# Optimization experiments

Measured on AMD Instinct MI355X. Metric: run time of the kernel, lower is better.

The kernel has to match this reference:

```python
import jax, jax.numpy as jnp
from jax import lax
import numpy as np

EPS = 4e-3            # geoopt float32 ball boundary eps
MAXNORM = 1.0 - EPS   # c = 1 Poincare ball


def _norm(x):
    return jnp.sqrt(jnp.maximum(jnp.sum(x * x, axis=-1, keepdims=True), 1e-15))


def expmap0(u):
    n = _norm(u)
    return jnp.tanh(n) * u / n


def projx(x):
    n = _norm(x)
    return jnp.where(n > MAXNORM, x * (MAXNORM / n), x)


def mobius_add(x, y):
    x2 = jnp.sum(x * x, -1, keepdims=True)
    y2 = jnp.sum(y * y, -1, keepdims=True)
    xy = jnp.sum(x * y, -1, keepdims=True)
    num = (1.0 + 2.0 * xy + y2) * x + (1.0 - x2) * y
    den = 1.0 + 2.0 * xy + x2 * y2
    return num / jnp.maximum(den, 1e-15)


def mamba_layer(x, inW, convW, convb, xpW, dtW, dtb, A_log, Dp, outW):
    # x: [B,T,H]; inW: [2*Din,H]; convW: [Din,K]; xpW: [R+2N,Din]; dtW: [Din,R]
    B, T, H = x.shape
    Din, N = A_log.shape
    K = convW.shape[-1]
    R = dtW.shape[-1]
    xz = jnp.einsum('bth,dh->btd', x, inW)              # [B,T,2*Din]
    xr, z = jnp.split(xz, 2, axis=-1)
    xc = lax.conv_general_dilated(jnp.transpose(xr, (0, 2, 1)), convW[:, None, :],
                                  (1,), [(K - 1, 0)], feature_group_count=Din)
    u = jax.nn.silu(jnp.transpose(xc + convb[None, :, None], (0, 2, 1)))  # [B,T,Din]
    x_dbl = jnp.einsum('btd,ed->bte', u, xpW)           # [B,T,R+2N]
    dt_r, Bm, Cm = x_dbl[..., :R], x_dbl[..., R:R + N], x_dbl[..., R + N:]
    dt = jax.nn.softplus(jnp.einsum('btr,dr->btd', dt_r, dtW) + dtb)      # [B,T,Din]
    A = -jnp.exp(A_log)                                 # [Din,N]
    dA = jnp.exp(dt[..., None] * A)                     # [B,T,Din,N]
    dBu = dt[..., None] * Bm[:, :, None, :] * u[..., None]

    def step(h, ins):
        dA_t, dBu_t, C_t = ins
        h = dA_t * h + dBu_t                            # [B,Din,N]
        return h, jnp.einsum('bdn,bn->bd', h, C_t)

    h0 = jnp.zeros((B, Din, N), x.dtype)
    _, ys = lax.scan(step, h0, (jnp.moveaxis(dA, 1, 0), jnp.moveaxis(dBu, 1, 0), jnp.moveaxis(Cm, 1, 0)))
    y = jnp.moveaxis(ys, 0, 1) + Dp * u                 # [B,T,Din]
    return jnp.einsum('btd,hd->bth', y * jax.nn.silu(z), outW)


def _encode(xs, inp_W, inp_b, in_proj_W, conv_W, conv_b, xproj_W, dt_W, dt_b, A_log, D_skip, out_W, outp_W, outp_b):
    # xs: [4,B,T,1]; params carry leading branch dim 4, then layer dim 3
    def branch(x, iW, ib, ipW, cW, cb, xpW, dW, db, Al, Dp, oW, opW, opb):
        h = jnp.einsum('bti,hi->bth', x, iW) + ib
        for l in range(ipW.shape[0]):
            h = mamba_layer(h, ipW[l], cW[l], cb[l], xpW[l], dW[l], db[l], Al[l], Dp[l], oW[l])
        return jnp.tanh(jnp.einsum('bth,eh->bte', h, opW) + opb)
    return jax.vmap(branch)(xs, inp_W, inp_b, in_proj_W, conv_W, conv_b, xproj_W, dt_W, dt_b, A_log, D_skip, out_W, outp_W, outp_b)


def setup_inputs() -> dict:
    key = jax.random.key(0)
    ks = jax.random.split(key, 24)
    Br, B, T, H, Din, N, K, R, E, L = 4, 32, 1024, 64, 128, 16, 4, 4, 32, 3

    def rn(k, shape, s=0.05):
        return jax.random.normal(k, shape, jnp.float32) * s

    A_init = jnp.log(jnp.arange(1, N + 1, dtype=jnp.float32))
    return {
        'trend': jax.random.normal(ks[0], (B, T, 1), jnp.float32),
        'seasonal_weekly': jax.random.normal(ks[1], (B, T, 1), jnp.float32),
        'seasonal_daily': jax.random.normal(ks[2], (B, T, 1), jnp.float32),
        'residual': jax.random.normal(ks[3], (B, T, 1), jnp.float32),
        'inp_W': rn(ks[4], (Br, H, 1), 0.5),
        'inp_b': rn(ks[5], (Br, H)),
        'in_proj_W': rn(ks[6], (Br, L, 2 * Din, H)),
        'conv_W': rn(ks[7], (Br, L, Din, K), 0.2),
        'conv_b': rn(ks[8], (Br, L, Din)),
        'xproj_W': rn(ks[9], (Br, L, R + 2 * N, Din)),
        'dt_W': rn(ks[10], (Br, L, Din, R), 0.2),
        'dt_b': rn(ks[11], (Br, L, Din), 0.5) - 4.0,  # softplus(dt_b) small
        'A_log': jnp.tile(A_init, (Br, L, Din, 1)) + rn(ks[12], (Br, L, Din, N), 0.01),
        'D_skip': jnp.ones((Br, L, Din), jnp.float32) + rn(ks[13], (Br, L, Din), 0.01),
        'out_W': rn(ks[14], (Br, L, H, Din)),
        'outp_W': rn(ks[15], (Br, E, H)),
        'outp_b': rn(ks[16], (Br, E)),
    }


def reference(trend, seasonal_weekly, seasonal_daily, residual, inp_W, inp_b, in_proj_W, conv_W, conv_b, xproj_W, dt_W, dt_b, A_log, D_skip, out_W, outp_W, outp_b):
    xs = jnp.stack([trend, seasonal_weekly, seasonal_daily, residual], 0)  # [4,B,T,1]
    z = _encode(xs, inp_W, inp_b, in_proj_W, conv_W, conv_b, xproj_W, dt_W, dt_b, A_log, D_skip, out_W, outp_W, outp_b)  # [4,B,T,E]
    zh = projx(expmap0(z))
    t, w, d, r = zh[0], zh[1], zh[2], zh[3]
    comb = projx(mobius_add(mobius_add(t, mobius_add(w, d)), r))
    # stacked [trend_h, weekly_h, daily_h, residual_h, combined_h]
    return jnp.stack([t, w, d, r, comb], 0)
```

## Files before the change

kernel.cpp:

```cpp
#include <hip/hip_runtime.h>
#include <math.h>

#define TT 1024
#define DIN 128
#define HH 64
#define NN 16
#define EE 32
#define LL 3
#define BB 32

__device__ __forceinline__ float siluf(float x) { return x / (1.f + __expf(-x)); }

typedef __attribute__((ext_vector_type(8))) short bf16x8;
typedef __attribute__((ext_vector_type(4))) float f32x4;

__device__ __forceinline__ void split2(float x, ushort& hi, ushort& lo) {
  unsigned u = __float_as_uint(x);
  hi = (ushort)(u >> 16);
  float rem = x - __uint_as_float((u >> 16) << 16);
  lo = (ushort)(__float_as_uint(rem) >> 16);
}

__global__ __launch_bounds__(256) void k_xz(
    const float* __restrict__ x0, const float* __restrict__ x1,
    const float* __restrict__ x2, const float* __restrict__ x3,
    const float* __restrict__ h, const float* __restrict__ inprojW,
    const float* __restrict__ inpW, const float* __restrict__ inpb,
    float* __restrict__ xr, float* __restrict__ zb, int br0, int l) {
  __shared__ __align__(16) ushort Hh[64][72], Hl[64][72];
  __shared__ __align__(16) ushort Wh[64][72], Wl[64][72];
  const int tid = threadIdx.x;
  const int b  = blockIdx.y;
  const int t0 = blockIdx.x * 64;
  const int n0 = blockIdx.z * 64;
  const int br = br0 + (b >> 5);
  const float* Wg = inprojW + (size_t)((br * LL + l) * 2 * DIN + n0) * HH;
  const float* Hg = h + ((size_t)b * TT + t0) * HH;
  {
    int row = tid >> 2, c0 = (tid & 3) * 16;
    float xv = 0.f;
    if (l == 0) {
      int bb = b & 31;
      const float* xp = (br == 0) ? x0 : (br == 1) ? x1 : (br == 2) ? x2 : x3;
      xv = xp[bb * TT + t0 + row];
    }
    #pragma unroll
    for (int q = 0; q < 4; ++q) {
      float4 hv;
      if (l == 0) {
        float4 w4 = *(const float4*)(inpW + br * HH + c0 + q * 4);
        float4 b4 = *(const float4*)(inpb + br * HH + c0 + q * 4);
        hv.x = xv * w4.x + b4.x; hv.y = xv * w4.y + b4.y;
        hv.z = xv * w4.z + b4.z; hv.w = xv * w4.w + b4.w;
      } else {
        hv = *(const float4*)(Hg + (size_t)row * HH + c0 + q * 4);
      }
      ushort h0,h1,h2,h3,l0,l1,l2,l3;
      split2(hv.x,h0,l0); split2(hv.y,h1,l1); split2(hv.z,h2,l2); split2(hv.w,h3,l3);
      *(ushort4*)&Hh[row][c0 + q*4] = make_ushort4(h0,h1,h2,h3);
      *(ushort4*)&Hl[row][c0 + q*4] = make_ushort4(l0,l1,l2,l3);
      float4 wv = *(const float4*)(Wg + (size_t)row * HH + c0 + q * 4);
      split2(wv.x,h0,l0); split2(wv.y,h1,l1); split2(wv.z,h2,l2); split2(wv.w,h3,l3);
      *(ushort4*)&Wh[row][c0 + q*4] = make_ushort4(h0,h1,h2,h3);
      *(ushort4*)&Wl[row][c0 + q*4] = make_ushort4(l0,l1,l2,l3);
    }
  }
  __syncthreads();
  const int wave = tid >> 6, lane = tid & 63;
  const int quad = lane >> 4, l16 = lane & 15;
  const int nsub = (wave & 1) * 32, tsub = (wave >> 1) * 32;
  f32x4 acc[2][2] = {};
  #pragma unroll
  for (int k0 = 0; k0 < 64; k0 += 32) {
    bf16x8 Ah[2], Al[2], Bh[2], Bl[2];
    #pragma unroll
    for (int i = 0; i < 2; ++i) {
      Ah[i] = *(const bf16x8*)&Wh[nsub + i*16 + l16][k0 + quad*8];
      Al[i] = *(const bf16x8*)&Wl[nsub + i*16 + l16][k0 + quad*8];
      Bh[i] = *(const bf16x8*)&Hh[tsub + i*16 + l16][k0 + quad*8];
      Bl[i] = *(const bf16x8*)&Hl[tsub + i*16 + l16][k0 + quad*8];
    }
    #pragma unroll
    for (int i = 0; i < 2; ++i)
      #pragma unroll
      for (int j = 0; j < 2; ++j) {
        acc[i][j] = __builtin_amdgcn_mfma_f32_16x16x32_bf16(Ah[i], Bh[j], acc[i][j], 0, 0, 0);
        acc[i][j] = __builtin_amdgcn_mfma_f32_16x16x32_bf16(Ah[i], Bl[j], acc[i][j], 0, 0, 0);
        acc[i][j] = __builtin_amdgcn_mfma_f32_16x16x32_bf16(Al[i], Bh[j], acc[i][j], 0, 0, 0);
      }
  }
  #pragma unroll
  for (int i = 0; i < 2; ++i) {
    #pragma unroll
    for (int r = 0; r < 4; ++r) {
      int n = n0 + nsub + i*16 + quad*4 + r;
      float* dst = (n < DIN) ? (xr + ((size_t)b * DIN + n) * TT)
                             : (zb + ((size_t)b * DIN + (n - DIN)) * TT);
      #pragma unroll
      for (int j = 0; j < 2; ++j)
        dst[t0 + tsub + j*16 + l16] = acc[i][j][r];
    }
  }
}

__global__ __launch_bounds__(256) void k_xdbl(
    const float* __restrict__ xr, const float* __restrict__ convW,
    const float* __restrict__ convb, const float* __restrict__ xprojW,
    const float* __restrict__ dtW, const float* __restrict__ dtb,
    float* __restrict__ u, float* __restrict__ dt,
    float* __restrict__ Bm, float* __restrict__ Cm,
    int br0, int l) {
  __shared__ __align__(16) float Xr[16][72];
  __shared__ __align__(16) float As2[32][68];
  __shared__ __align__(16) float Ws2[32][48];
  __shared__ __align__(16) float Xs[40][68];
  const int tid = threadIdx.x;
  const int b  = blockIdx.y;
  const int t0 = blockIdx.x * 64;
  const int br = br0 + (b >> 5);
  const float* W = xprojW + (size_t)((br * LL + l) * 36) * DIN;
  const int rowk = tid >> 4, c4 = tid & 15;
  const int wave = tid >> 6, lane = tid & 63;
  const int quad = lane >> 4, l16 = lane & 15;
  const int tw = wave * 16;
  f32x4 acc[3] = {};
  for (int k0 = 0; k0 < DIN; k0 += 32) {
    #pragma unroll
    for (int ks = 0; ks < 32; ks += 16) {
      __syncthreads();
      {
        const float* src = xr + ((size_t)b * DIN + k0 + ks + rowk) * TT + t0;
        *(float4*)&Xr[rowk][4 + c4 * 4] = *(const float4*)(src + c4 * 4);
        if (tid < 16) {
          float4 hv = make_float4(0.f, 0.f, 0.f, 0.f);
          if (t0 > 0) hv = *(const float4*)(xr + ((size_t)b * DIN + k0 + ks + tid) * TT + t0 - 4);
          *(float4*)&Xr[tid][0] = hv;
        }
      }
      __syncthreads();
      {
        int d = k0 + ks + rowk;
        const float* w = convW + (size_t)((br * LL + l) * DIN + d) * 4;
        float w0 = w[0], w1 = w[1], w2 = w[2], w3 = w[3];
        float cb = convb[(br * LL + l) * DIN + d];
        int i0 = c4 * 4;
        float o[4];
        #pragma unroll
        for (int q = 0; q < 4; ++q) {
          int j = i0 + q;
          float a = Xr[rowk][j+1]*w0 + Xr[rowk][j+2]*w1 + Xr[rowk][j+3]*w2 + Xr[rowk][j+4]*w3 + cb;
          o[q] = siluf(a);
        }
        float4 uo = make_float4(o[0], o[1], o[2], o[3]);
        *(float4*)&As2[ks + rowk][i0] = uo;
        *(float4*)(u + ((size_t)b * DIN + d) * TT + t0 + i0) = uo;
      }
    }
    for (int idx = tid; idx < 1536; idx += 256) {
      int jj = idx >> 5, kk = idx & 31;
      Ws2[kk][jj] = (jj < 36) ? W[(size_t)jj * DIN + k0 + kk] : 0.f;
    }
    __syncthreads();
    ushort bh[8], bl[8];
    #pragma unroll
    for (int j = 0; j < 8; ++j) {
      float v = As2[quad * 8 + j][tw + l16];
      split2(v, bh[j], bl[j]);
    }
    bf16x8 Bh = *(bf16x8*)bh, Bl = *(bf16x8*)bl;
    #pragma unroll
    for (int nf = 0; nf < 3; ++nf) {
      ushort wh[8], wl[8];
      #pragma unroll
      for (int j = 0; j < 8; ++j) {
        float v = Ws2[quad * 8 + j][nf * 16 + l16];
        split2(v, wh[j], wl[j]);
      }
      bf16x8 Wh = *(bf16x8*)wh, Wl = *(bf16x8*)wl;
      acc[nf] = __builtin_amdgcn_mfma_f32_16x16x32_bf16(Wh, Bh, acc[nf], 0, 0, 0);
      acc[nf] = __builtin_amdgcn_mfma_f32_16x16x32_bf16(Wh, Bl, acc[nf], 0, 0, 0);
      acc[nf] = __builtin_amdgcn_mfma_f32_16x16x32_bf16(Wl, Bh, acc[nf], 0, 0, 0);
    }
  }
  __syncthreads();
  #pragma unroll
  for (int nf = 0; nf < 3; ++nf) {
    #pragma unroll
    for (int r = 0; r < 4; ++r) {
      int n = nf * 16 + quad * 4 + r;
      if (n < 40) Xs[n][tw + l16] = acc[nf][r];
    }
  }
  __syncthreads();
  {
    int n = tid >> 4, i0 = (tid & 15) * 4;
    *(float4*)(Bm + ((size_t)b * NN + n) * TT + t0 + i0) = *(float4*)&Xs[4 + n][i0];
    *(float4*)(Cm + ((size_t)b * NN + n) * TT + t0 + i0) = *(float4*)&Xs[20 + n][i0];
  }
  {
    int d = tid >> 1, half = tid & 1;
    const float* wd = dtW + (size_t)((br * LL + l) * DIN + d) * 4;
    float w0 = wd[0], w1 = wd[1], w2 = wd[2], w3 = wd[3];
    float bias = dtb[(br * LL + l) * DIN + d];
    float* dtp = dt + ((size_t)b * DIN + d) * TT + t0 + half * 32;
    #pragma unroll
    for (int g8 = 0; g8 < 8; ++g8) {
      float o[4];
      #pragma unroll
      for (int q = 0; q < 4; ++q) {
        int i = half * 32 + g8 * 4 + q;
        float s = Xs[0][i]*w0 + Xs[1][i]*w1 + Xs[2][i]*w2 + Xs[3][i]*w3 + bias;
        float e = __expf(-fabsf(s));
        o[q] = fmaxf(s, 0.f) + __logf(1.f + e);
      }
      *(float4*)(dtp + g8*4) = make_float4(o[0], o[1], o[2], o[3]);
    }
  }
}

__global__ __launch_bounds__(256) void k_scan1(
    float* dtc, const float* __restrict__ u,
    const float* __restrict__ Bm, const float* __restrict__ Cm,
    const float* __restrict__ A_log, const float* __restrict__ D_skip,
    float* __restrict__ Hloc, float* __restrict__ g, int br0, int l) {
  __shared__ __align__(16) float Bl[16][68];
  __shared__ __align__(16) float Cl[16][68];
  const int bx  = blockIdx.x;
  const int b   = bx >> 5;
  const int rem = bx & 31;
  const int c   = rem >> 1;
  const int dh  = rem & 1;
  const int tid = threadIdx.x;
  {
    int row = tid >> 4, cc = (tid & 15) * 4;
    *(float4*)&Bl[row][cc] = *(const float4*)(Bm + ((size_t)b * NN + row) * TT + c * 64 + cc);
    *(float4*)&Cl[row][cc] = *(const float4*)(Cm + ((size_t)b * NN + row) * TT + c * 64 + cc);
  }
  __syncthreads();
  const int d  = dh * 64 + (tid >> 2);
  const int n0 = (tid & 3) * 4;
  const int br = br0 + (b >> 5);
  const int wbase = (br * LL + l) * DIN + d;
  float Ac[4];
  #pragma unroll
  for (int j = 0; j < 4; ++j) Ac[j] = -__expf(A_log[(size_t)wbase * NN + n0 + j]);
  float Dp = D_skip[wbase];
  float* dtp = dtc + ((size_t)b * DIN + d) * TT + c * 64;
  const float* up = u + ((size_t)b * DIN + d) * TT + c * 64;
  float* gp = g + ((size_t)b * DIN + d) * TT + c * 64;
  float hst[4] = {0.f, 0.f, 0.f, 0.f};
  float sd = 0.f;
  for (int t0 = 0; t0 < 64; t0 += 8) {
    float4 dq0 = *(const float4*)(dtp + t0);
    float4 dq1 = *(const float4*)(dtp + t0 + 4);
    float4 uq0 = *(const float4*)(up + t0);
    float4 uq1 = *(const float4*)(up + t0 + 4);
    float dts[8] = {dq0.x, dq0.y, dq0.z, dq0.w, dq1.x, dq1.y, dq1.z, dq1.w};
    float us[8]  = {uq0.x, uq0.y, uq0.z, uq0.w, uq1.x, uq1.y, uq1.z, uq1.w};
    float Bs[4][8], Cr[4][8];
    #pragma unroll
    for (int j = 0; j < 4; ++j) {
      float4 b0 = *(const float4*)&Bl[n0 + j][t0];
      float4 b1 = *(const float4*)&Bl[n0 + j][t0 + 4];
      Bs[j][0]=b0.x; Bs[j][1]=b0.y; Bs[j][2]=b0.z; Bs[j][3]=b0.w;
      Bs[j][4]=b1.x; Bs[j][5]=b1.y; Bs[j][6]=b1.z; Bs[j][7]=b1.w;
      float4 c0 = *(const float4*)&Cl[n0 + j][t0];
      float4 c1 = *(const float4*)&Cl[n0 + j][t0 + 4];
      Cr[j][0]=c0.x; Cr[j][1]=c0.y; Cr[j][2]=c0.z; Cr[j][3]=c0.w;
      Cr[j][4]=c1.x; Cr[j][5]=c1.y; Cr[j][6]=c1.z; Cr[j][7]=c1.w;
    }
    float yo[8], cd8[8];
    #pragma unroll
    for (int s = 0; s < 8; ++s) {
      float dtv = dts[s], uv = us[s];
      sd += dtv;
      cd8[s] = sd;
      float du = dtv * uv;
      float acc = 0.f;
      #pragma unroll
      for (int j = 0; j < 4; ++j) {
        float dA = __expf(dtv * Ac[j]);
        hst[j] = dA * hst[j] + du * Bs[j][s];
        acc += hst[j] * Cr[j][s];
      }
      acc += __shfl_xor(acc, 1, 4);
      acc += __shfl_xor(acc, 2, 4);
      yo[s] = acc + Dp * uv;
    }
    if ((tid & 3) == 0) {
      *(float4*)(gp + t0)      = make_float4(yo[0], yo[1], yo[2], yo[3]);
      *(float4*)(gp + t0 + 4)  = make_float4(yo[4], yo[5], yo[6], yo[7]);
      *(float4*)(dtp + t0)     = make_float4(cd8[0], cd8[1], cd8[2], cd8[3]);
      *(float4*)(dtp + t0 + 4) = make_float4(cd8[4], cd8[5], cd8[6], cd8[7]);
    }
  }
  *(float4*)(Hloc + (((size_t)b * DIN + d) * 16 + c) * 16 + n0) =
      make_float4(hst[0], hst[1], hst[2], hst[3]);
}

__global__ __launch_bounds__(256) void k_scan2(
    const float* __restrict__ cd, const float* __restrict__ Cm,
    const float* __restrict__ A_log, const float* __restrict__ Hloc,
    float* __restrict__ g, int br0, int l) {
  __shared__ __align__(16) float Cl[16][68];
  __shared__ __align__(16) float HinL[32][16];
  const int bx  = blockIdx.x;
  const int b   = bx >> 6;
  const int rem = bx & 63;
  const int c   = rem >> 2;
  const int dq  = rem & 3;
  const int tid = threadIdx.x;
  const int br  = br0 + (b >> 5);
  if (c == 0) return;
  {
    int row = tid >> 4, cc = (tid & 15) * 4;
    *(float4*)&Cl[row][cc] = *(const float4*)(Cm + ((size_t)b * NN + row) * TT + c * 64 + cc);
  }
  {
    int dloc = tid >> 3;
    int n0 = (tid & 7) * 2;
    int d = dq * 32 + dloc;
    int wbase = (br * LL + l) * DIN + d;
    float a0 = -__expf(A_log[(size_t)wbase * NN + n0]);
    float a1 = -__expf(A_log[(size_t)wbase * NN + n0 + 1]);
    float h0 = 0.f, h1 = 0.f;
    const float* cdrow = cd + ((size_t)b * DIN + d) * TT;
    const float* hlb = Hloc + ((size_t)b * DIN + d) * 256;
    for (int cc = 0; cc < c; ++cc) {
      float sdv = cdrow[cc * 64 + 63];
      float2 hl = *(const float2*)(hlb + cc * 16 + n0);
      h0 = __expf(a0 * sdv) * h0 + hl.x;
      h1 = __expf(a1 * sdv) * h1 + hl.y;
    }
    HinL[dloc][n0] = h0;
    HinL[dloc][n0 + 1] = h1;
  }
  __syncthreads();
  const int dloc = tid >> 3, tg = tid & 7;
  const int d  = dq * 32 + dloc;
  const float* al = A_log + (size_t)((br * LL + l) * DIN + d) * NN;
  float Ac16[16];
  #pragma unroll
  for (int n = 0; n < 16; ++n) Ac16[n] = -__expf(al[n]);
  size_t off = ((size_t)b * DIN + d) * TT + c * 64 + tg * 8;
  float4 cd0 = *(const float4*)(cd + off);
  float4 cd1 = *(const float4*)(cd + off + 4);
  float cd8[8] = {cd0.x, cd0.y, cd0.z, cd0.w, cd1.x, cd1.y, cd1.z, cd1.w};
  float* gp = g + off;
  float4 y0 = *(float4*)gp;
  float4 y1 = *(float4*)(gp + 4);
  float y8[8] = {y0.x, y0.y, y0.z, y0.w, y1.x, y1.y, y1.z, y1.w};
  const int tbase = tg * 8;
  #pragma unroll
  for (int n = 0; n < 16; ++n) {
    float hv = HinL[dloc][n];
    float an = Ac16[n];
    #pragma unroll
    for (int s = 0; s < 8; ++s)
      y8[s] += Cl[n][tbase + s] * __expf(an * cd8[s]) * hv;
  }
  *(float4*)gp       = make_float4(y8[0], y8[1], y8[2], y8[3]);
  *(float4*)(gp + 4) = make_float4(y8[4], y8[5], y8[6], y8[7]);
}

__global__ __launch_bounds__(256) void k_out(
    const float* __restrict__ graw, const float* __restrict__ zb,
    const float* __restrict__ outW, float* __restrict__ h, int br0, int l) {
  __shared__ __align__(16) ushort Ah_[64][72], Al_[64][72];
  __shared__ __align__(16) ushort Bh_[64][72], Bl_[64][72];
  const int tid = threadIdx.x;
  const int b  = blockIdx.y;
  const int t0 = blockIdx.x * 64;
  const int br = br0 + (b >> 5);
  const float* Wg = outW + (size_t)((br * LL + l) * HH) * DIN;
  const int wave = tid >> 6, lane = tid & 63;
  const int quad = lane >> 4, l16 = lane & 15;
  const int hsub = (wave & 1) * 32, tsub = (wave >> 1) * 32;
  f32x4 acc[2][2] = {};
  for (int k0 = 0; k0 < DIN; k0 += 64) {
    __syncthreads();
    {
      int row = tid >> 2, c0 = (tid & 3) * 16;
      #pragma unroll
      for (int q = 0; q < 4; ++q) {
        float4 wv = *(const float4*)(Wg + (size_t)row * DIN + k0 + c0 + q * 4);
        ushort h0,h1,h2,h3,l0,l1,l2,l3;
        split2(wv.x,h0,l0); split2(wv.y,h1,l1); split2(wv.z,h2,l2); split2(wv.w,h3,l3);
        *(ushort4*)&Ah_[row][c0 + q*4] = make_ushort4(h0,h1,h2,h3);
        *(ushort4*)&Al_[row][c0 + q*4] = make_ushort4(l0,l1,l2,l3);
        size_t off = ((size_t)b * DIN + k0 + row) * TT + t0 + c0 + q * 4;
        float4 gv = *(const float4*)(graw + off);
        float4 zv = *(const float4*)(zb + off);
        float a0 = gv.x * siluf(zv.x), a1 = gv.y * siluf(zv.y);
        float a2 = gv.z * siluf(zv.z), a3 = gv.w * siluf(zv.w);
        split2(a0,h0,l0); split2(a1,h1,l1); split2(a2,h2,l2); split2(a3,h3,l3);
        *(ushort4*)&Bh_[row][c0 + q*4] = make_ushort4(h0,h1,h2,h3);
        *(ushort4*)&Bl_[row][c0 + q*4] = make_ushort4(l0,l1,l2,l3);
      }
    }
    __syncthreads();
    #pragma unroll
    for (int kk = 0; kk < 64; kk += 32) {
      bf16x8 Ahf[2], Alf[2], Bhf[2], Blf[2];
      #pragma unroll
      for (int i = 0; i < 2; ++i) {
        Ahf[i] = *(const bf16x8*)&Ah_[hsub + i*16 + l16][kk + quad*8];
        Alf[i] = *(const bf16x8*)&Al_[hsub + i*16 + l16][kk + quad*8];
        Bhf[i] = *(const bf16x8*)&Bh_[tsub + i*16 + l16][kk + quad*8];
        Blf[i] = *(const bf16x8*)&Bl_[tsub + i*16 + l16][kk + quad*8];
      }
      #pragma unroll
      for (int i = 0; i < 2; ++i)
        #pragma unroll
        for (int j = 0; j < 2; ++j) {
          acc[i][j] = __builtin_amdgcn_mfma_f32_16x16x32_bf16(Ahf[i], Bhf[j], acc[i][j], 0, 0, 0);
          acc[i][j] = __builtin_amdgcn_mfma_f32_16x16x32_bf16(Ahf[i], Blf[j], acc[i][j], 0, 0, 0);
          acc[i][j] = __builtin_amdgcn_mfma_f32_16x16x32_bf16(Alf[i], Bhf[j], acc[i][j], 0, 0, 0);
        }
    }
  }
  #pragma unroll
  for (int i = 0; i < 2; ++i) {
    int hh0 = hsub + i*16 + quad*4;
    #pragma unroll
    for (int j = 0; j < 2; ++j) {
      int t = t0 + tsub + j*16 + l16;
      *(f32x4*)(h + ((size_t)b * TT + t) * HH + hh0) = acc[i][j];
    }
  }
}

__global__ __launch_bounds__(256) void k_ze(
    const float* __restrict__ h, const float* __restrict__ outpW,
    const float* __restrict__ outpb, float* __restrict__ ze, int br0) {
  __shared__ __align__(16) float As[16][132];
  __shared__ __align__(16) float Ws[16][36];
  __shared__ __align__(16) float Cs[128][36];
  const int tid = threadIdx.x;
  const int b  = blockIdx.y;
  const int t0 = blockIdx.x * 128;
  const int br = br0 + (b >> 5);
  const float* W = outpW + (size_t)br * EE * HH;
  float acc[4][4] = {};
  const int ti = tid & 31, ni = tid >> 5;
  for (int k0 = 0; k0 < HH; k0 += 16) {
    __syncthreads();
    {
      int i = tid >> 1, kq = (tid & 1) * 8;
      const float* src = h + ((size_t)b * TT + t0 + i) * HH + k0 + kq;
      float4 a0 = *(const float4*)src;
      float4 a1 = *(const float4*)(src + 4);
      As[kq+0][i]=a0.x; As[kq+1][i]=a0.y; As[kq+2][i]=a0.z; As[kq+3][i]=a0.w;
      As[kq+4][i]=a1.x; As[kq+5][i]=a1.y; As[kq+6][i]=a1.z; As[kq+7][i]=a1.w;
    }
    for (int idx = tid; idx < 512; idx += 256) {
      int jj = idx >> 4, kk = idx & 15;
      Ws[kk][jj] = W[(size_t)jj * HH + k0 + kk];
    }
    __syncthreads();
    #pragma unroll
    for (int kk = 0; kk < 16; ++kk) {
      float4 a = *(const float4*)&As[kk][ti * 4];
      float4 w = *(const float4*)&Ws[kk][ni * 4];
      acc[0][0] += a.x*w.x; acc[0][1] += a.x*w.y; acc[0][2] += a.x*w.z; acc[0][3] += a.x*w.w;
      acc[1][0] += a.y*w.x; acc[1][1] += a.y*w.y; acc[1][2] += a.y*w.z; acc[1][3] += a.y*w.w;
      acc[2][0] += a.z*w.x; acc[2][1] += a.z*w.y; acc[2][2] += a.z*w.z; acc[2][3] += a.z*w.w;
      acc[3][0] += a.w*w.x; acc[3][1] += a.w*w.y; acc[3][2] += a.w*w.z; acc[3][3] += a.w*w.w;
    }
  }
  __syncthreads();
  float bj[4];
  #pragma unroll
  for (int c = 0; c < 4; ++c) bj[c] = outpb[br * EE + ni*4 + c];
  #pragma unroll
  for (int r = 0; r < 4; ++r)
    #pragma unroll
    for (int c = 0; c < 4; ++c)
      Cs[ti*4+r][ni*4+c] = tanhf(acc[r][c] + bj[c]);
  __syncthreads();
  int i = tid >> 1, j16 = (tid & 1) * 16;
  float* dst = ze + (((size_t)(br0 * 32 + b)) * TT + t0 + i) * EE + j16;
  #pragma unroll
  for (int q = 0; q < 4; ++q)
    *(float4*)(dst + q*4) = *(float4*)&Cs[i][j16 + q*4];
}

__device__ __forceinline__ void mobius_add32(const float* x, const float* y, float* o) {
  float x2 = 0.f, y2 = 0.f, xy = 0.f;
  #pragma unroll
  for (int i = 0; i < 32; ++i) { x2 += x[i]*x[i]; y2 += y[i]*y[i]; xy += x[i]*y[i]; }
  float ca  = 1.f + 2.f*xy + y2;
  float cb  = 1.f - x2;
  float den = 1.f + 2.f*xy + x2*y2;
  float inv = 1.f / fmaxf(den, 1e-15f);
  #pragma unroll
  for (int i = 0; i < 32; ++i) o[i] = (ca*x[i] + cb*y[i]) * inv;
}

__global__ __launch_bounds__(256) void k_hyper(const float* __restrict__ ze,
                                               float* __restrict__ out) {
  int idx = blockIdx.x * 256 + threadIdx.x;
  int b = idx >> 10, t = idx & 1023;
  float v[4][32];
  #pragma unroll
  for (int br = 0; br < 4; ++br) {
    const float* p = ze + (((size_t)br * BB + b) * TT + t) * EE;
    float s = 0.f;
    #pragma unroll
    for (int e = 0; e < 32; ++e) { v[br][e] = p[e]; s += v[br][e]*v[br][e]; }
    float nr = sqrtf(fmaxf(s, 1e-15f));
    float sc = tanhf(nr) / nr;
    float s2 = 0.f;
    #pragma unroll
    for (int e = 0; e < 32; ++e) { v[br][e] *= sc; s2 += v[br][e]*v[br][e]; }
    float n2 = sqrtf(fmaxf(s2, 1e-15f));
    if (n2 > 0.996f) {
      float sc2 = 0.996f / n2;
      #pragma unroll
      for (int e = 0; e < 32; ++e) v[br][e] *= sc2;
    }
    float* o = out + (((size_t)br * BB + b) * TT + t) * EE;
    #pragma unroll
    for (int e = 0; e < 32; ++e) o[e] = v[br][e];
  }
  float m1[32], m2[32];
  mobius_add32(v[1], v[2], m1);
  mobius_add32(v[0], m1, m2);
  mobius_add32(m2, v[3], m1);
  float s = 0.f;
  #pragma unroll
  for (int e = 0; e < 32; ++e) s += m1[e]*m1[e];
  float n = sqrtf(fmaxf(s, 1e-15f));
  if (n > 0.996f) {
    float sc = 0.996f / n;
    #pragma unroll
    for (int e = 0; e < 32; ++e) m1[e] *= sc;
  }
  float* o = out + (((size_t)4 * BB + b) * TT + t) * EE;
  #pragma unroll
  for (int e = 0; e < 32; ++e) o[e] = m1[e];
}

extern "C" void kernel_launch(void* const* d_in, const int* in_sizes, int n_in,
                              void* d_out, int out_size, void* d_ws, size_t ws_size,
                              hipStream_t stream) {
  const float* xs0 = (const float*)d_in[0];
  const float* xs1 = (const float*)d_in[1];
  const float* xs2 = (const float*)d_in[2];
  const float* xs3 = (const float*)d_in[3];
  const float* inpW   = (const float*)d_in[4];
  const float* inpb   = (const float*)d_in[5];
  const float* iprojW = (const float*)d_in[6];
  const float* convW  = (const float*)d_in[7];
  const float* convb  = (const float*)d_in[8];
  const float* xprojW = (const float*)d_in[9];
  const float* dtW    = (const float*)d_in[10];
  const float* dtb    = (const float*)d_in[11];
  const float* A_log  = (const float*)d_in[12];
  const float* D_skip = (const float*)d_in[13];
  const float* outW   = (const float*)d_in[14];
  const float* outpW  = (const float*)d_in[15];
  const float* outpb  = (const float*)d_in[16];
  float* out = (float*)d_out;
  float* ws  = (float*)d_ws;

  const size_t zeF = (size_t)4 * BB * TT * EE;
  const size_t perBl = 65536 + 4 * 131072 + 2 * 16384;
  auto needBytes = [&](int NB) { return (zeF + (size_t)NB * 32 * perBl) * 4; };
  int NB = 4;
  if (needBytes(4) > ws_size) NB = 2;
  if (NB == 2 && needBytes(2) > ws_size) NB = 1;
  const int nbl = NB * 32;

  float* ze = ws;
  float* h  = ze + zeF;
  float* xr = h  + (size_t)nbl * 65536;
  float* zb = xr + (size_t)nbl * 131072;
  float* u  = zb + (size_t)nbl * 131072;
  float* dt = u  + (size_t)nbl * 131072;
  float* Bm = dt + (size_t)nbl * 131072;
  float* Cm = Bm + (size_t)nbl * 16384;
  float* g  = xr;
  float* Hloc = h;

  for (int br0 = 0; br0 < 4; br0 += NB) {
    for (int l = 0; l < LL; ++l) {
      k_xz   <<<dim3(16, nbl, 4), 256, 0, stream>>>(xs0, xs1, xs2, xs3, h, iprojW,
                                                    inpW, inpb, xr, zb, br0, l);
      k_xdbl <<<dim3(16, nbl), 256, 0, stream>>>(xr, convW, convb, xprojW, dtW, dtb,
                                                 u, dt, Bm, Cm, br0, l);
      k_scan1<<<nbl * 32, 256, 0, stream>>>(dt, u, Bm, Cm, A_log, D_skip, Hloc, g, br0, l);
      k_scan2<<<nbl * 64, 256, 0, stream>>>(dt, Cm, A_log, Hloc, g, br0, l);
      k_out  <<<dim3(16, nbl), 256, 0, stream>>>(g, zb, outW, h, br0, l);
    }
    k_ze<<<dim3(8, nbl), 256, 0, stream>>>(h, outpW, outpb, ze, br0);
  }
  k_hyper<<<BB * TT / 256, 256, 0, stream>>>(ze, out);
}
```

Before: 1.083 ms.

## Reuse H tile across all in_proj column blocks and stop writing cumulative dt

After: 1.010 ms. -6.7%, faster.

```diff
diff --git a/kernel.cpp b/kernel.cpp
--- a/kernel.cpp
+++ b/kernel.cpp
@@ -32,12 +32,10 @@
   const int tid = threadIdx.x;
   const int b  = blockIdx.y;
   const int t0 = blockIdx.x * 64;
-  const int n0 = blockIdx.z * 64;
   const int br = br0 + (b >> 5);
-  const float* Wg = inprojW + (size_t)((br * LL + l) * 2 * DIN + n0) * HH;
   const float* Hg = h + ((size_t)b * TT + t0) * HH;
-  {
-    int row = tid >> 2, c0 = (tid & 3) * 16;
+  const int row = tid >> 2, c0 = (tid & 3) * 16;
+  {
     float xv = 0.f;
     if (l == 0) {
       int bb = b & 31;
@@ -59,47 +57,57 @@
       split2(hv.x,h0,l0); split2(hv.y,h1,l1); split2(hv.z,h2,l2); split2(hv.w,h3,l3);
       *(ushort4*)&Hh[row][c0 + q*4] = make_ushort4(h0,h1,h2,h3);
       *(ushort4*)&Hl[row][c0 + q*4] = make_ushort4(l0,l1,l2,l3);
-      float4 wv = *(const float4*)(Wg + (size_t)row * HH + c0 + q * 4);
-      split2(wv.x,h0,l0); split2(wv.y,h1,l1); split2(wv.z,h2,l2); split2(wv.w,h3,l3);
-      *(ushort4*)&Wh[row][c0 + q*4] = make_ushort4(h0,h1,h2,h3);
-      *(ushort4*)&Wl[row][c0 + q*4] = make_ushort4(l0,l1,l2,l3);
-    }
-  }
-  __syncthreads();
+    }
+  }
   const int wave = tid >> 6, lane = tid & 63;
   const int quad = lane >> 4, l16 = lane & 15;
   const int nsub = (wave & 1) * 32, tsub = (wave >> 1) * 32;
-  f32x4 acc[2][2] = {};
-  #pragma unroll
-  for (int k0 = 0; k0 < 64; k0 += 32) {
-    bf16x8 Ah[2], Al[2], Bh[2], Bl[2];
+  for (int n0 = 0; n0 < 2 * DIN; n0 += 64) {
+    const float* Wg = inprojW + (size_t)((br * LL + l) * 2 * DIN + n0) * HH;
+    {
+      #pragma unroll
+      for (int q = 0; q < 4; ++q) {
+        float4 wv = *(const float4*)(Wg + (size_t)row * HH + c0 + q * 4);
+        ushort h0,h1,h2,h3,l0,l1,l2,l3;
+        split2(wv.x,h0,l0); split2(wv.y,h1,l1); split2(wv.z,h2,l2); split2(wv.w,h3,l3);
+        *(ushort4*)&Wh[row][c0 + q*4] = make_ushort4(h0,h1,h2,h3);
+        *(ushort4*)&Wl[row][c0 + q*4] = make_ushort4(l0,l1,l2,l3);
+      }
+    }
+    __syncthreads();
+    f32x4 acc[2][2] = {};
+    #pragma unroll
+    for (int k0 = 0; k0 < 64; k0 += 32) {
+      bf16x8 Ah[2], Al[2], Bh[2], Bl[2];
+      #pragma unroll
+      for (int i = 0; i < 2; ++i) {
+        Ah[i] = *(const bf16x8*)&Wh[nsub + i*16 + l16][k0 + quad*8];
+        Al[i] = *(const bf16x8*)&Wl[nsub + i*16 + l16][k0 + quad*8];
+        Bh[i] = *(const bf16x8*)&Hh[tsub + i*16 + l16][k0 + quad*8];
+        Bl[i] = *(const bf16x8*)&Hl[tsub + i*16 + l16][k0 + quad*8];
+      }
+      #pragma unroll
+      for (int i = 0; i < 2; ++i)
+        #pragma unroll
+        for (int j = 0; j < 2; ++j) {
+          acc[i][j] = __builtin_amdgcn_mfma_f32_16x16x32_bf16(Ah[i], Bh[j], acc[i][j], 0, 0, 0);
+          acc[i][j] = __builtin_amdgcn_mfma_f32_16x16x32_bf16(Ah[i], Bl[j], acc[i][j], 0, 0, 0);
+          acc[i][j] = __builtin_amdgcn_mfma_f32_16x16x32_bf16(Al[i], Bh[j], acc[i][j], 0, 0, 0);
+        }
+    }
     #pragma unroll
     for (int i = 0; i < 2; ++i) {
-      Ah[i] = *(const bf16x8*)&Wh[nsub + i*16 + l16][k0 + quad*8];
-      Al[i] = *(const bf16x8*)&Wl[nsub + i*16 + l16][k0 + quad*8];
-      Bh[i] = *(const bf16x8*)&Hh[tsub + i*16 + l16][k0 + quad*8];
-      Bl[i] = *(const bf16x8*)&Hl[tsub + i*16 + l16][k0 + quad*8];
-    }
-    #pragma unroll
-    for (int i = 0; i < 2; ++i)
-      #pragma unroll
-      for (int j = 0; j < 2; ++j) {
-        acc[i][j] = __builtin_amdgcn_mfma_f32_16x16x32_bf16(Ah[i], Bh[j], acc[i][j], 0, 0, 0);
-        acc[i][j] = __builtin_amdgcn_mfma_f32_16x16x32_bf16(Ah[i], Bl[j], acc[i][j], 0, 0, 0);
-        acc[i][j] = __builtin_amdgcn_mfma_f32_16x16x32_bf16(Al[i], Bh[j], acc[i][j], 0, 0, 0);
-      }
-  }
-  #pragma unroll
-  for (int i = 0; i < 2; ++i) {
-    #pragma unroll
-    for (int r = 0; r < 4; ++r) {
-      int n = n0 + nsub + i*16 + quad*4 + r;
-      float* dst = (n < DIN) ? (xr + ((size_t)b * DIN + n) * TT)
-                             : (zb + ((size_t)b * DIN + (n - DIN)) * TT);
-      #pragma unroll
-      for (int j = 0; j < 2; ++j)
-        dst[t0 + tsub + j*16 + l16] = acc[i][j][r];
-    }
+      #pragma unroll
+      for (int r = 0; r < 4; ++r) {
+        int n = n0 + nsub + i*16 + quad*4 + r;
+        float* dst = (n < DIN) ? (xr + ((size_t)b * DIN + n) * TT)
+                               : (zb + ((size_t)b * DIN + (n - DIN)) * TT);
+        #pragma unroll
+        for (int j = 0; j < 2; ++j)
+          dst[t0 + tsub + j*16 + l16] = acc[i][j][r];
+      }
+    }
+    __syncthreads();
   }
 }
 
@@ -219,10 +227,11 @@
 }
 
 __global__ __launch_bounds__(256) void k_scan1(
-    float* dtc, const float* __restrict__ u,
+    const float* __restrict__ dtc, const float* __restrict__ u,
     const float* __restrict__ Bm, const float* __restrict__ Cm,
     const float* __restrict__ A_log, const float* __restrict__ D_skip,
-    float* __restrict__ Hloc, float* __restrict__ g, int br0, int l) {
+    float* __restrict__ Hloc, float* __restrict__ g, float* __restrict__ sdt,
+    int br0, int l) {
   __shared__ __align__(16) float Bl[16][68];
   __shared__ __align__(16) float Cl[16][68];
   const int bx  = blockIdx.x;
@@ -245,7 +254,7 @@
   #pragma unroll
   for (int j = 0; j < 4; ++j) Ac[j] = -__expf(A_log[(size_t)wbase * NN + n0 + j]);
   float Dp = D_skip[wbase];
-  float* dtp = dtc + ((size_t)b * DIN + d) * TT + c * 64;
+  const float* dtp = dtc + ((size_t)b * DIN + d) * TT + c * 64;
   const float* up = u + ((size_t)b * DIN + d) * TT + c * 64;
   float* gp = g + ((size_t)b * DIN + d) * TT + c * 64;
   float hst[4] = {0.f, 0.f, 0.f, 0.f};
@@ -269,12 +278,11 @@
       Cr[j][0]=c0.x; Cr[j][1]=c0.y; Cr[j][2]=c0.z; Cr[j][3]=c0.w;
       Cr[j][4]=c1.x; Cr[j][5]=c1.y; Cr[j][6]=c1.z; Cr[j][7]=c1.w;
     }
-    float yo[8], cd8[8];
+    float yo[8];
     #pragma unroll
     for (int s = 0; s < 8; ++s) {
       float dtv = dts[s], uv = us[s];
       sd += dtv;
-      cd8[s] = sd;
       float du = dtv * uv;
       float acc = 0.f;
       #pragma unroll
@@ -288,21 +296,21 @@
       yo[s] = acc + Dp * uv;
     }
     if ((tid & 3) == 0) {
-      *(float4*)(gp + t0)      = make_float4(yo[0], yo[1], yo[2], yo[3]);
-      *(float4*)(gp + t0 + 4)  = make_float4(yo[4], yo[5], yo[6], yo[7]);
-      *(float4*)(dtp + t0)     = make_float4(cd8[0], cd8[1], cd8[2], cd8[3]);
-      *(float4*)(dtp + t0 + 4) = make_float4(cd8[4], cd8[5], cd8[6], cd8[7]);
+      *(float4*)(gp + t0)     = make_float4(yo[0], yo[1], yo[2], yo[3]);
+      *(float4*)(gp + t0 + 4) = make_float4(yo[4], yo[5], yo[6], yo[7]);
     }
   }
   *(float4*)(Hloc + (((size_t)b * DIN + d) * 16 + c) * 16 + n0) =
       make_float4(hst[0], hst[1], hst[2], hst[3]);
+  if ((tid & 3) == 0) sdt[((size_t)b * DIN + d) * 16 + c] = sd;
 }
 
 __global__ __launch_bounds__(256) void k_scan2(
-    const float* __restrict__ cd, const float* __restrict__ Cm,
+    const float* __restrict__ dtc, const float* __restrict__ Cm,
     const float* __restrict__ A_log, const float* __restrict__ Hloc,
-    float* __restrict__ g, int br0, int l) {
+    const float* __restrict__ sdt, float* __restrict__ g, int br0, int l) {
   __shared__ __align__(16) float Cl[16][68];
+  __shared__ __align__(16) float Dl[32][68];
   __shared__ __align__(16) float HinL[32][16];
   const int bx  = blockIdx.x;
   const int b   = bx >> 6;
@@ -316,18 +324,23 @@
     int row = tid >> 4, cc = (tid & 15) * 4;
     *(float4*)&Cl[row][cc] = *(const float4*)(Cm + ((size_t)b * NN + row) * TT + c * 64 + cc);
   }
-  {
-    int dloc = tid >> 3;
+  const int dloc = tid >> 3, tg = tid & 7;
+  const int d  = dq * 32 + dloc;
+  {
+    const float* dp = dtc + ((size_t)b * DIN + d) * TT + c * 64 + tg * 8;
+    *(float4*)&Dl[dloc][tg * 8]     = *(const float4*)dp;
+    *(float4*)&Dl[dloc][tg * 8 + 4] = *(const float4*)(dp + 4);
+  }
+  {
     int n0 = (tid & 7) * 2;
-    int d = dq * 32 + dloc;
     int wbase = (br * LL + l) * DIN + d;
     float a0 = -__expf(A_log[(size_t)wbase * NN + n0]);
     float a1 = -__expf(A_log[(size_t)wbase * NN + n0 + 1]);
     float h0 = 0.f, h1 = 0.f;
-    const float* cdrow = cd + ((size_t)b * DIN + d) * TT;
+    const float* sp  = sdt + ((size_t)b * DIN + d) * 16;
     const float* hlb = Hloc + ((size_t)b * DIN + d) * 256;
     for (int cc = 0; cc < c; ++cc) {
-      float sdv = cdrow[cc * 64 + 63];
+      float sdv = sp[cc];
       float2 hl = *(const float2*)(hlb + cc * 16 + n0);
       h0 = __expf(a0 * sdv) * h0 + hl.x;
       h1 = __expf(a1 * sdv) * h1 + hl.y;
@@ -336,16 +349,18 @@
     HinL[dloc][n0 + 1] = h1;
   }
   __syncthreads();
-  const int dloc = tid >> 3, tg = tid & 7;
-  const int d  = dq * 32 + dloc;
+  float cd8[8];
+  {
+    float run = 0.f;
+    for (int t = 0; t < tg * 8; ++t) run += Dl[dloc][t];
+    #pragma unroll
+    for (int s = 0; s < 8; ++s) { run += Dl[dloc][tg * 8 + s]; cd8[s] = run; }
+  }
   const float* al = A_log + (size_t)((br * LL + l) * DIN + d) * NN;
   float Ac16[16];
   #pragma unroll
   for (int n = 0; n < 16; ++n) Ac16[n] = -__expf(al[n]);
   size_t off = ((size_t)b * DIN + d) * TT + c * 64 + tg * 8;
-  float4 cd0 = *(const float4*)(cd + off);
-  float4 cd1 = *(const float4*)(cd + off + 4);
-  float cd8[8] = {cd0.x, cd0.y, cd0.z, cd0.w, cd1.x, cd1.y, cd1.z, cd1.w};
   float* gp = g + off;
   float4 y0 = *(float4*)gp;
   float4 y1 = *(float4*)(gp + 4);
@@ -565,7 +580,7 @@
   float* ws  = (float*)d_ws;
 
   const size_t zeF = (size_t)4 * BB * TT * EE;
-  const size_t perBl = 65536 + 4 * 131072 + 2 * 16384;
+  const size_t perBl = 65536 + 4 * 131072 + 2 * 16384 + 2048;
   auto needBytes = [&](int NB) { return (zeF + (size_t)NB * 32 * perBl) * 4; };
   int NB = 4;
   if (needBytes(4) > ws_size) NB = 2;
@@ -580,17 +595,19 @@
   float* dt = u  + (size_t)nbl * 131072;
   float* Bm = dt + (size_t)nbl * 131072;
   float* Cm = Bm + (size_t)nbl * 16384;
+  float* sdt = Cm + (size_t)nbl * 16384;
   float* g  = xr;
   float* Hloc = h;
 
   for (int br0 = 0; br0 < 4; br0 += NB) {
     for (int l = 0; l < LL; ++l) {
-      k_xz   <<<dim3(16, nbl, 4), 256, 0, stream>>>(xs0, xs1, xs2, xs3, h, iprojW,
-                                                    inpW, inpb, xr, zb, br0, l);
+      k_xz   <<<dim3(16, nbl), 256, 0, stream>>>(xs0, xs1, xs2, xs3, h, iprojW,
+                                                 inpW, inpb, xr, zb, br0, l);
       k_xdbl <<<dim3(16, nbl), 256, 0, stream>>>(xr, convW, convb, xprojW, dtW, dtb,
                                                  u, dt, Bm, Cm, br0, l);
-      k_scan1<<<nbl * 32, 256, 0, stream>>>(dt, u, Bm, Cm, A_log, D_skip, Hloc, g, br0, l);
-      k_scan2<<<nbl * 64, 256, 0, stream>>>(dt, Cm, A_log, Hloc, g, br0, l);
+      k_scan1<<<nbl * 32, 256, 0, stream>>>(dt, u, Bm, Cm, A_log, D_skip,
+                                            Hloc, g, sdt, br0, l);
+      k_scan2<<<nbl * 64, 256, 0, stream>>>(dt, Cm, A_log, Hloc, sdt, g, br0, l);
       k_out  <<<dim3(16, nbl), 256, 0, stream>>>(g, zb, outW, h, br0, l);
     }
     k_ze<<<dim3(8, nbl), 256, 0, stream>>>(h, outpW, outpb, ze, br0);
```
